# Kernel optimization log

Measured on AMD Instinct MI355X. Metric: run time of the kernel, lower is better.

The kernel has to match this reference:

```python
import jax, jax.numpy as jnp
import numpy as np

N = 100_000   # number of sparse points
C = 128       # channels
K3 = 27       # 3x3x3 kernel offsets


def sparse_conv(x, nbr, W, b):
    """Minkowski-style sparse conv: gather-GEMM-scatter.
    x:   [N, Cin] point features
    nbr: [N, K3] neighbor index per kernel offset; index N -> missing (zero row)
    W:   [K3, Cin, Cout], b: [Cout]
    """
    x_pad = jnp.concatenate([x, jnp.zeros((1, x.shape[1]), x.dtype)], axis=0)

    def step(acc, wk_nk):
        Wk, nk = wk_nk                      # Wk: [Cin,Cout], nk: [N]
        return acc + x_pad[nk] @ Wk, None   # gather + GEMM, accumulate

    acc0 = jnp.broadcast_to(b, (x.shape[0], W.shape[2])).astype(x.dtype)
    acc, _ = jax.lax.scan(step, acc0, (W, nbr.T))
    return acc


def setup_inputs() -> dict:
    key = jax.random.key(0)
    ks = jax.random.split(key, 12)
    Ch = C // 2

    def w(k, shape, fan_in):
        return jax.random.normal(k, shape, dtype=jnp.float32) / np.sqrt(fan_in)

    x = jax.random.normal(ks[0], (N, C), dtype=jnp.float32)
    # neighbor map; value N means "no neighbor" (maps to zero-padded row)
    nbr = jax.random.randint(ks[1], (N, K3), 0, N + 1, dtype=jnp.int32)

    return {
        "x": x,
        "nbr": nbr,
        "W00": w(ks[2], (K3, C, Ch), K3 * C),   # conv0_0: kxkxk, C -> C/2
        "b00": jnp.zeros((Ch,), jnp.float32),
        "W01": w(ks[3], (K3, Ch, Ch), K3 * Ch),  # conv0_1: kxkxk, C/2 -> C/2
        "b01": jnp.zeros((Ch,), jnp.float32),
        "W10": w(ks[4], (C, Ch), C),             # conv1_0: 1x1x1, C -> C/2
        "b10": jnp.zeros((Ch,), jnp.float32),
        "W11": w(ks[5], (K3, Ch, Ch), K3 * Ch),  # conv1_1: kxkxk, C/2 -> C/2
        "b11": jnp.zeros((Ch,), jnp.float32),
        "W12": w(ks[6], (Ch, Ch), Ch),           # conv1_2: 1x1x1, C/2 -> C/2
        "b12": jnp.zeros((Ch,), jnp.float32),
    }


def reference(x, nbr, W00, b00, W01, b01, W10, b10, W11, b11, W12, b12):
    # branch 0: conv -> relu -> conv
    h0 = jax.nn.relu(sparse_conv(x, nbr, W00, b00))
    out0 = sparse_conv(h0, nbr, W01, b01)
    # branch 1: 1x1 conv -> relu -> conv -> relu -> 1x1 conv
    h1 = jax.nn.relu(x @ W10 + b10)
    h1 = jax.nn.relu(sparse_conv(h1, nbr, W11, b11))
    out1 = h1 @ W12 + b12
    # concat channels, residual add
    return jnp.concatenate([out0, out1], axis=1) + x
```

## Files before the change

kernel.cpp:

```cpp
#include <hip/hip_runtime.h>
#include <hip/hip_bf16.h>
#include <stdint.h>

typedef __bf16 bf16x8 __attribute__((ext_vector_type(8)));
typedef float  f32x4  __attribute__((ext_vector_type(4)));

#define MFMA(A, B, C) __builtin_amdgcn_mfma_f32_16x16x32_bf16((A), (B), (C), 0, 0, 0)

#define LDS_BARRIER() asm volatile("s_waitcnt lgkmcnt(0)\n\ts_barrier" ::: "memory")

static __device__ __forceinline__ unsigned short f2b(float f) {
    union { float f; unsigned int u; } v; v.f = f;
    return (unsigned short)((v.u + 0x7FFFu + ((v.u >> 16) & 1u)) >> 16);
}

__global__ __launch_bounds__(256) void convert_kernel(
    const float* __restrict__ x, unsigned short* __restrict__ xb,
    unsigned short* __restrict__ hb, int N) {
    long long i = (long long)blockIdx.x * blockDim.x + threadIdx.x;
    long long base = i * 4;
    long long nx = (long long)N * 128;
    long long total = nx + 128;
    if (base >= total) return;
    if (base < nx) {
        float4 v = *(const float4*)(x + base);
        ushort4 o;
        o.x = f2b(v.x); o.y = f2b(v.y); o.z = f2b(v.z); o.w = f2b(v.w);
        *(ushort4*)(xb + base) = o;
    } else {
        ushort4 z = make_ushort4(0, 0, 0, 0);
        *(ushort4*)(xb + base) = z;
        *(ushort4*)(hb + base) = z;
    }
}

__global__ __launch_bounds__(256) void pack_kernel(
    const float* __restrict__ W00, const float* __restrict__ W01,
    const float* __restrict__ W10, const float* __restrict__ W11,
    const float* __restrict__ W12,
    unsigned short* __restrict__ wp00, unsigned short* __restrict__ wpC,
    unsigned short* __restrict__ wp10, unsigned short* __restrict__ wp12) {
    int g = blockIdx.x * blockDim.x + threadIdx.x;
    const float* W; int cinSteps; int which;
    if (g < 27648)      { W = W00; cinSteps = 4; which = 0; }
    else if (g < 41472) { g -= 27648; W = W01; cinSteps = 2; which = 1; }
    else if (g < 55296) { g -= 41472; W = W11; cinSteps = 2; which = 2; }
    else if (g < 56320) { g -= 55296; W = W10; cinSteps = 4; which = 3; }
    else if (g < 56832) { g -= 56320; W = W12; cinSteps = 2; which = 4; }
    else return;
    int lane = g & 63;
    int st   = g >> 6;
    int t    = st & 3;
    int s    = st >> 2;
    int q = lane >> 4, n16 = lane & 15;
    int k    = s / cinSteps;
    int cinb = (s % cinSteps) * 32;
    int Cin  = cinSteps * 32;
    int cout = t * 16 + n16;
    unsigned short o[8];
#pragma unroll
    for (int j = 0; j < 8; ++j) {
        float v = W[(size_t)(k * Cin + cinb + q * 8 + j) * 64 + cout];
        o[j] = f2b(v);
    }
    unsigned short* dst;
    if (which == 0)      dst = wp00 + (size_t)g * 8;
    else if (which == 1) dst = wpC + (size_t)k * 8192 +
                               ((size_t)(((s & 1) * 4 + t) * 64 + lane)) * 8;
    else if (which == 2) dst = wpC + (size_t)k * 8192 + 4096 +
                               ((size_t)(((s & 1) * 4 + t) * 64 + lane)) * 8;
    else if (which == 3) dst = wp10 + (size_t)g * 8;
    else                 dst = wp12 + (size_t)g * 8;
    *(ushort4*)(dst)     = make_ushort4(o[0], o[1], o[2], o[3]);
    *(ushort4*)(dst + 4) = make_ushort4(o[4], o[5], o[6], o[7]);
}

__global__ __launch_bounds__(256, 3) void passB_kernel(
    const unsigned short* __restrict__ xb, const int* __restrict__ nbr,
    const unsigned short* __restrict__ wp00, const unsigned short* __restrict__ wp10,
    const float* __restrict__ b00, const float* __restrict__ b10,
    unsigned short* __restrict__ hb, int N) {
    __shared__ __align__(16) unsigned short bbuf[2][4096];
    __shared__ __align__(16) int lds_idx[128 * 27];
    const int tid  = threadIdx.x;
    const int lane = tid & 63;
    const int wv   = tid >> 6;
    const int q = lane >> 4, n16 = lane & 15;
    const int rowbase = blockIdx.x * 128 + wv * 32;

    f32x4 acc0[2][4];
    f32x4 acc1[2][4];
#pragma unroll
    for (int rs = 0; rs < 2; ++rs)
#pragma unroll
        for (int t = 0; t < 4; ++t) { acc0[rs][t] = (f32x4)0.f; acc1[rs][t] = (f32x4)0.f; }

    int idxb[2], own[2];
#pragma unroll
    for (int rs = 0; rs < 2; ++rs) {
        idxb[rs] = (wv * 32 + rs * 16 + n16) * 27;
        own[rs]  = min(rowbase + rs * 16 + n16, N - 1);
    }

#pragma unroll
    for (int ph = 0; ph < 2; ++ph) {
        const int choff = ph * 64;
        int4 br[2];
#pragma unroll
        for (int j = 0; j < 2; ++j)
            br[j] = *(const int4*)(wp00 + ph * 4096 + j * 2048 + tid * 8);
        if (ph == 0) {
            long long gbase = (long long)blockIdx.x * 128 * 27;
            long long lim = (long long)N * 27 - 1;
            for (int i = tid; i < 3456; i += 256) {
                long long gi = gbase + i; if (gi > lim) gi = lim;
                lds_idx[i] = nbr[gi];
            }
        }
#pragma unroll
        for (int j = 0; j < 2; ++j) *(int4*)(&bbuf[0][j * 2048 + tid * 8]) = br[j];
        __syncthreads();

        bf16x8 Da[2][2], Db[2][2], Dc[2][2];
#pragma unroll
        for (int rs = 0; rs < 2; ++rs) {
            const unsigned short* p0 =
                xb + (size_t)lds_idx[idxb[rs] + 0] * 128 + choff + q * 8;
            Da[rs][0] = *(const bf16x8*)(p0);
            Da[rs][1] = *(const bf16x8*)(p0 + 32);
            const unsigned short* p1 =
                xb + (size_t)lds_idx[idxb[rs] + 1] * 128 + choff + q * 8;
            Db[rs][0] = *(const bf16x8*)(p1);
            Db[rs][1] = *(const bf16x8*)(p1 + 32);
        }

        for (int k = 0; k < 27; ++k) {
            int buf = k & 1;
            if (k < 26) {
                const unsigned short* src = wp00 + ph * 4096 + (size_t)(k + 1) * 8192;
#pragma unroll
                for (int j = 0; j < 2; ++j)
                    br[j] = *(const int4*)(src + j * 2048 + tid * 8);
            }
#pragma unroll
            for (int rs = 0; rs < 2; ++rs) {
                int j2 = k + 2;
                int ii = (j2 < 27) ? lds_idx[idxb[rs] + j2] : own[rs];
                const unsigned short* p = xb + (size_t)ii * 128 + choff + q * 8;
                Dc[rs][0] = *(const bf16x8*)(p);
                Dc[rs][1] = *(const bf16x8*)(p + 32);
            }
            const unsigned short* lb = &bbuf[buf][0];
#pragma unroll
            for (int s2 = 0; s2 < 2; ++s2) {
#pragma unroll
                for (int t = 0; t < 4; ++t) {
                    bf16x8 B = *(const bf16x8*)(lb + (s2 * 4 + t) * 512 + lane * 8);
#pragma unroll
                    for (int rs = 0; rs < 2; ++rs)
                        acc0[rs][t] = MFMA(Da[rs][s2], B, acc0[rs][t]);
                }
            }
            if (k < 26) {
#pragma unroll
                for (int j = 0; j < 2; ++j)
                    *(int4*)(&bbuf[buf ^ 1][j * 2048 + tid * 8]) = br[j];
            }
#pragma unroll
            for (int rs = 0; rs < 2; ++rs)
#pragma unroll
                for (int s2 = 0; s2 < 2; ++s2) {
                    Da[rs][s2] = Db[rs][s2]; Db[rs][s2] = Dc[rs][s2];
                }
            LDS_BARRIER();
        }

#pragma unroll
        for (int s2 = 0; s2 < 2; ++s2) {
#pragma unroll
            for (int t = 0; t < 4; ++t) {
                bf16x8 B = *(const bf16x8*)(wp10 + ((ph * 2 + s2) * 4 + t) * 512 + lane * 8);
#pragma unroll
                for (int rs = 0; rs < 2; ++rs)
                    acc1[rs][t] = MFMA(Da[rs][s2], B, acc1[rs][t]);
            }
        }
    }

#pragma unroll
    for (int rs = 0; rs < 2; ++rs)
#pragma unroll
        for (int t = 0; t < 4; ++t) {
            int col = t * 16 + n16;
            float bb0 = b00[col], bb1 = b10[col];
#pragma unroll
            for (int r = 0; r < 4; ++r) {
                int row = rowbase + rs * 16 + q * 4 + r;
                if (row < N) {
                    hb[(size_t)row * 128 + col]      = f2b(fmaxf(acc0[rs][t][r] + bb0, 0.f));
                    hb[(size_t)row * 128 + 64 + col] = f2b(fmaxf(acc1[rs][t][r] + bb1, 0.f));
                }
            }
        }
}

__global__ __launch_bounds__(256, 3) void passC_kernel(
    const unsigned short* __restrict__ hb, const int* __restrict__ nbr,
    const float* __restrict__ x,
    const unsigned short* __restrict__ wpC, const unsigned short* __restrict__ wp12,
    const float* __restrict__ b01, const float* __restrict__ b11,
    const float* __restrict__ b12, float* __restrict__ out, int N) {
    __shared__ __align__(16) unsigned short bbuf[2][4096];
    __shared__ __align__(16) int lds_idx[128 * 27];
    const int tid  = threadIdx.x;
    const int lane = tid & 63;
    const int wv   = tid >> 6;
    const int q = lane >> 4, n16 = lane & 15;
    const int rowbase = blockIdx.x * 128 + wv * 32;

    int idxb[2];
#pragma unroll
    for (int rs = 0; rs < 2; ++rs) idxb[rs] = (wv * 32 + rs * 16 + n16) * 27;

    {
        int4 br[2];
#pragma unroll
        for (int j = 0; j < 2; ++j) br[j] = *(const int4*)(wpC + j * 2048 + tid * 8);
        {
            long long gbase = (long long)blockIdx.x * 128 * 27;
            long long lim = (long long)N * 27 - 1;
            for (int i = tid; i < 3456; i += 256) {
                long long gi = gbase + i; if (gi > lim) gi = lim;
                lds_idx[i] = nbr[gi];
            }
        }
#pragma unroll
        for (int j = 0; j < 2; ++j) *(int4*)(&bbuf[0][j * 2048 + tid * 8]) = br[j];
        __syncthreads();

        f32x4 accA[2][4];
#pragma unroll
        for (int rs = 0; rs < 2; ++rs)
#pragma unroll
            for (int t = 0; t < 4; ++t) accA[rs][t] = (f32x4)0.f;

        bf16x8 Da[2][2], Db[2][2], Dc[2][2];
#pragma unroll
        for (int rs = 0; rs < 2; ++rs) {
            const unsigned short* p0 = hb + (size_t)lds_idx[idxb[rs] + 0] * 128 + q * 8;
            Da[rs][0] = *(const bf16x8*)(p0);
            Da[rs][1] = *(const bf16x8*)(p0 + 32);
            const unsigned short* p1 = hb + (size_t)lds_idx[idxb[rs] + 1] * 128 + q * 8;
            Db[rs][0] = *(const bf16x8*)(p1);
            Db[rs][1] = *(const bf16x8*)(p1 + 32);
        }

        for (int k = 0; k < 27; ++k) {
            int buf = k & 1;
            if (k < 26) {
                const unsigned short* src = wpC + (size_t)(k + 1) * 8192;
#pragma unroll
                for (int j = 0; j < 2; ++j)
                    br[j] = *(const int4*)(src + j * 2048 + tid * 8);
            }
#pragma unroll
            for (int rs = 0; rs < 2; ++rs) {
                int j2 = min(k + 2, 26);
                const unsigned short* p =
                    hb + (size_t)lds_idx[idxb[rs] + j2] * 128 + q * 8;
                Dc[rs][0] = *(const bf16x8*)(p);
                Dc[rs][1] = *(const bf16x8*)(p + 32);
            }
            const unsigned short* lb = &bbuf[buf][0];
#pragma unroll
            for (int s2 = 0; s2 < 2; ++s2) {
#pragma unroll
                for (int t = 0; t < 4; ++t) {
                    bf16x8 B = *(const bf16x8*)(lb + (s2 * 4 + t) * 512 + lane * 8);
#pragma unroll
                    for (int rs = 0; rs < 2; ++rs)
                        accA[rs][t] = MFMA(Da[rs][s2], B, accA[rs][t]);
                }
            }
            if (k < 26) {
#pragma unroll
                for (int j = 0; j < 2; ++j)
                    *(int4*)(&bbuf[buf ^ 1][j * 2048 + tid * 8]) = br[j];
            }
#pragma unroll
            for (int rs = 0; rs < 2; ++rs)
#pragma unroll
                for (int s2 = 0; s2 < 2; ++s2) {
                    Da[rs][s2] = Db[rs][s2]; Db[rs][s2] = Dc[rs][s2];
                }
            LDS_BARRIER();
        }

#pragma unroll
        for (int rs = 0; rs < 2; ++rs)
#pragma unroll
            for (int t = 0; t < 4; ++t) {
                int col = t * 16 + n16;
                float bo = b01[col];
#pragma unroll
                for (int r = 0; r < 4; ++r) {
                    int row = rowbase + rs * 16 + q * 4 + r;
                    if (row < N) {
                        float xv = __builtin_nontemporal_load(x + (size_t)row * 128 + col);
                        __builtin_nontemporal_store(accA[rs][t][r] + bo + xv,
                                                    out + (size_t)row * 128 + col);
                    }
                }
            }
    }

    {
        int4 br[2];
#pragma unroll
        for (int j = 0; j < 2; ++j)
            br[j] = *(const int4*)(wpC + 4096 + j * 2048 + tid * 8);
#pragma unroll
        for (int j = 0; j < 2; ++j) *(int4*)(&bbuf[0][j * 2048 + tid * 8]) = br[j];
        __syncthreads();

        f32x4 accT[2][4];
#pragma unroll
        for (int rs = 0; rs < 2; ++rs)
#pragma unroll
            for (int t = 0; t < 4; ++t) accT[rs][t] = (f32x4)0.f;

        bf16x8 Da[2][2], Db[2][2], Dc[2][2];
#pragma unroll
        for (int rs = 0; rs < 2; ++rs) {
            const unsigned short* p0 =
                hb + (size_t)lds_idx[idxb[rs] + 0] * 128 + 64 + q * 8;
            Da[rs][0] = *(const bf16x8*)(p0);
            Da[rs][1] = *(const bf16x8*)(p0 + 32);
            const unsigned short* p1 =
                hb + (size_t)lds_idx[idxb[rs] + 1] * 128 + 64 + q * 8;
            Db[rs][0] = *(const bf16x8*)(p1);
            Db[rs][1] = *(const bf16x8*)(p1 + 32);
        }

        for (int k = 0; k < 27; ++k) {
            int buf = k & 1;
            if (k < 26) {
                const unsigned short* src = wpC + 4096 + (size_t)(k + 1) * 8192;
#pragma unroll
                for (int j = 0; j < 2; ++j)
                    br[j] = *(const int4*)(src + j * 2048 + tid * 8);
            }
#pragma unroll
            for (int rs = 0; rs < 2; ++rs) {
                int j2 = min(k + 2, 26);
                const unsigned short* p =
                    hb + (size_t)lds_idx[idxb[rs] + j2] * 128 + 64 + q * 8;
                Dc[rs][0] = *(const bf16x8*)(p);
                Dc[rs][1] = *(const bf16x8*)(p + 32);
            }
            const unsigned short* lb = &bbuf[buf][0];
#pragma unroll
            for (int s2 = 0; s2 < 2; ++s2) {
#pragma unroll
                for (int t = 0; t < 4; ++t) {
                    bf16x8 B = *(const bf16x8*)(lb + (s2 * 4 + t) * 512 + lane * 8);
#pragma unroll
                    for (int rs = 0; rs < 2; ++rs)
                        accT[rs][t] = MFMA(Da[rs][s2], B, accT[rs][t]);
                }
            }
            if (k < 26) {
#pragma unroll
                for (int j = 0; j < 2; ++j)
                    *(int4*)(&bbuf[buf ^ 1][j * 2048 + tid * 8]) = br[j];
            }
#pragma unroll
            for (int rs = 0; rs < 2; ++rs)
#pragma unroll
                for (int s2 = 0; s2 < 2; ++s2) {
                    Da[rs][s2] = Db[rs][s2]; Db[rs][s2] = Dc[rs][s2];
                }
            LDS_BARRIER();
        }

        unsigned short* myl = (wv < 3) ? ((unsigned short*)lds_idx + wv * 2304)
                                       : &bbuf[0][0];
#pragma unroll
        for (int rs = 0; rs < 2; ++rs)
#pragma unroll
            for (int t = 0; t < 4; ++t) {
                int col = t * 16 + n16;
                float bt = b11[col];
#pragma unroll
                for (int r = 0; r < 4; ++r) {
                    float tv = fmaxf(accT[rs][t][r] + bt, 0.f);
                    myl[(rs * 16 + q * 4 + r) * 72 + col] = f2b(tv);
                }
            }

        f32x4 accO1[2][4];
#pragma unroll
        for (int rs = 0; rs < 2; ++rs)
#pragma unroll
            for (int t = 0; t < 4; ++t) accO1[rs][t] = (f32x4)0.f;
#pragma unroll
        for (int s2 = 0; s2 < 2; ++s2) {
#pragma unroll
            for (int t = 0; t < 4; ++t) {
                bf16x8 B = *(const bf16x8*)(wp12 + s2 * 2048 + t * 512 + lane * 8);
#pragma unroll
                for (int rs = 0; rs < 2; ++rs) {
                    bf16x8 A = *(const bf16x8*)(myl + (rs * 16 + n16) * 72 + s2 * 32 + q * 8);
                    accO1[rs][t] = MFMA(A, B, accO1[rs][t]);
                }
            }
        }
#pragma unroll
        for (int rs = 0; rs < 2; ++rs)
#pragma unroll
            for (int t = 0; t < 4; ++t) {
                int col = t * 16 + n16;
                float bo = b12[col];
#pragma unroll
                for (int r = 0; r < 4; ++r) {
                    int row = rowbase + rs * 16 + q * 4 + r;
                    if (row < N) {
                        float xv = __builtin_nontemporal_load(x + (size_t)row * 128 + 64 + col);
                        __builtin_nontemporal_store(accO1[rs][t][r] + bo + xv,
                                                    out + (size_t)row * 128 + 64 + col);
                    }
                }
            }
    }
}

extern "C" void kernel_launch(void* const* d_in, const int* in_sizes, int n_in,
                              void* d_out, int out_size, void* d_ws, size_t ws_size,
                              hipStream_t stream) {
    const float* x   = (const float*)d_in[0];
    const int*   nbr = (const int*)d_in[1];
    const float* W00 = (const float*)d_in[2];
    const float* b00 = (const float*)d_in[3];
    const float* W01 = (const float*)d_in[4];
    const float* b01 = (const float*)d_in[5];
    const float* W10 = (const float*)d_in[6];
    const float* b10 = (const float*)d_in[7];
    const float* W11 = (const float*)d_in[8];
    const float* b11 = (const float*)d_in[9];
    const float* W12 = (const float*)d_in[10];
    const float* b12 = (const float*)d_in[11];
    float* out = (float*)d_out;
    int N = in_sizes[0] / 128;

    char* ws = (char*)d_ws;
    size_t cur = 0;
    unsigned short* xb  = (unsigned short*)(ws + cur); cur += (size_t)(N + 1) * 128 * 2;
    unsigned short* hb  = (unsigned short*)(ws + cur); cur += (size_t)(N + 1) * 128 * 2;
    unsigned short* wp00 = (unsigned short*)(ws + cur); cur += 27648 * 8 * 2;
    unsigned short* wpC  = (unsigned short*)(ws + cur); cur += (size_t)27 * 8192 * 2;
    unsigned short* wp10 = (unsigned short*)(ws + cur); cur += 8192 * 2;
    unsigned short* wp12 = (unsigned short*)(ws + cur); cur += 4096 * 2;

    long long cvt_groups = ((long long)N * 128 + 128) / 4;
    int cvt_blocks = (int)((cvt_groups + 255) / 256);
    convert_kernel<<<cvt_blocks, 256, 0, stream>>>(x, xb, hb, N);
    pack_kernel<<<222, 256, 0, stream>>>(W00, W01, W10, W11, W12,
                                         wp00, wpC, wp10, wp12);
    int nstrips = (N + 127) / 128;
    passB_kernel<<<nstrips, 256, 0, stream>>>(xb, nbr, wp00, wp10, b00, b10, hb, N);
    passC_kernel<<<nstrips, 256, 0, stream>>>(hb, nbr, x, wpC, wp12,
                                              b01, b11, b12, out, N);
}
```

Before: 417.8 us.

## Widen passB tiles to 256 rows and full 128 channels in one pass

passB now processes 256 rows per block, 64 per wave, and covers all 128 input channels in a single k-loop instead of two 64-channel phases. Each gathered neighbor row is read once at full width, and each weight slice is staged once per block for twice as many rows. The gather prefetch depth drops from two offsets ahead to one. Register use rises (16 accumulators of each kind plus 32 fragment vectors), so occupancy is lowered to 2 blocks per CU, and the block count halves, which may hurt latency hiding.

```diff
diff --git a/kernel.cpp b/kernel.cpp
--- a/kernel.cpp
+++ b/kernel.cpp
@@ -75,120 +75,107 @@
     *(ushort4*)(dst + 4) = make_ushort4(o[4], o[5], o[6], o[7]);
 }
 
-__global__ __launch_bounds__(256, 3) void passB_kernel(
+__global__ __launch_bounds__(256, 2) void passB_kernel(
     const unsigned short* __restrict__ xb, const int* __restrict__ nbr,
     const unsigned short* __restrict__ wp00, const unsigned short* __restrict__ wp10,
     const float* __restrict__ b00, const float* __restrict__ b10,
     unsigned short* __restrict__ hb, int N) {
-    __shared__ __align__(16) unsigned short bbuf[2][4096];
-    __shared__ __align__(16) int lds_idx[128 * 27];
+    __shared__ __align__(16) unsigned short bbuf[2][8192];
+    __shared__ __align__(16) int lds_idx[256 * 27];
     const int tid  = threadIdx.x;
     const int lane = tid & 63;
     const int wv   = tid >> 6;
     const int q = lane >> 4, n16 = lane & 15;
-    const int rowbase = blockIdx.x * 128 + wv * 32;
-
-    f32x4 acc0[2][4];
-    f32x4 acc1[2][4];
-#pragma unroll
-    for (int rs = 0; rs < 2; ++rs)
+    const int rowbase = blockIdx.x * 256 + wv * 64;
+
+    int4 br[4];
+#pragma unroll
+    for (int j = 0; j < 4; ++j) br[j] = *(const int4*)(wp00 + j * 2048 + tid * 8);
+    {
+        long long gbase = (long long)blockIdx.x * 256 * 27;
+        long long lim = (long long)N * 27 - 1;
+        for (int i = tid; i < 6912; i += 256) {
+            long long gi = gbase + i; if (gi > lim) gi = lim;
+            lds_idx[i] = nbr[gi];
+        }
+    }
+#pragma unroll
+    for (int j = 0; j < 4; ++j) *(int4*)(&bbuf[0][j * 2048 + tid * 8]) = br[j];
+    __syncthreads();
+
+    f32x4 acc0[4][4];
+    f32x4 acc1[4][4];
+#pragma unroll
+    for (int rs = 0; rs < 4; ++rs)
 #pragma unroll
         for (int t = 0; t < 4; ++t) { acc0[rs][t] = (f32x4)0.f; acc1[rs][t] = (f32x4)0.f; }
 
-    int idxb[2], own[2];
-#pragma unroll
-    for (int rs = 0; rs < 2; ++rs) {
-        idxb[rs] = (wv * 32 + rs * 16 + n16) * 27;
+    int idxb[4], own[4];
+#pragma unroll
+    for (int rs = 0; rs < 4; ++rs) {
+        idxb[rs] = (wv * 64 + rs * 16 + n16) * 27;
         own[rs]  = min(rowbase + rs * 16 + n16, N - 1);
     }
 
-#pragma unroll
-    for (int ph = 0; ph < 2; ++ph) {
-        const int choff = ph * 64;
-        int4 br[2];
-#pragma unroll
-        for (int j = 0; j < 2; ++j)
-            br[j] = *(const int4*)(wp00 + ph * 4096 + j * 2048 + tid * 8);
-        if (ph == 0) {
-            long long gbase = (long long)blockIdx.x * 128 * 27;
-            long long lim = (long long)N * 27 - 1;
-            for (int i = tid; i < 3456; i += 256) {
-                long long gi = gbase + i; if (gi > lim) gi = lim;
-                lds_idx[i] = nbr[gi];
-            }
-        }
-#pragma unroll
-        for (int j = 0; j < 2; ++j) *(int4*)(&bbuf[0][j * 2048 + tid * 8]) = br[j];
-        __syncthreads();
-
-        bf16x8 Da[2][2], Db[2][2], Dc[2][2];
-#pragma unroll
-        for (int rs = 0; rs < 2; ++rs) {
-            const unsigned short* p0 =
-                xb + (size_t)lds_idx[idxb[rs] + 0] * 128 + choff + q * 8;
-            Da[rs][0] = *(const bf16x8*)(p0);
-            Da[rs][1] = *(const bf16x8*)(p0 + 32);
-            const unsigned short* p1 =
-                xb + (size_t)lds_idx[idxb[rs] + 1] * 128 + choff + q * 8;
-            Db[rs][0] = *(const bf16x8*)(p1);
-            Db[rs][1] = *(const bf16x8*)(p1 + 32);
-        }
-
-        for (int k = 0; k < 27; ++k) {
-            int buf = k & 1;
-            if (k < 26) {
-                const unsigned short* src = wp00 + ph * 4096 + (size_t)(k + 1) * 8192;
-#pragma unroll
-                for (int j = 0; j < 2; ++j)
-                    br[j] = *(const int4*)(src + j * 2048 + tid * 8);
-            }
-#pragma unroll
-            for (int rs = 0; rs < 2; ++rs) {
-                int j2 = k + 2;
-                int ii = (j2 < 27) ? lds_idx[idxb[rs] + j2] : own[rs];
-                const unsigned short* p = xb + (size_t)ii * 128 + choff + q * 8;
-                Dc[rs][0] = *(const bf16x8*)(p);
-                Dc[rs][1] = *(const bf16x8*)(p + 32);
-            }
-            const unsigned short* lb = &bbuf[buf][0];
-#pragma unroll
-            for (int s2 = 0; s2 < 2; ++s2) {
-#pragma unroll
-                for (int t = 0; t < 4; ++t) {
-                    bf16x8 B = *(const bf16x8*)(lb + (s2 * 4 + t) * 512 + lane * 8);
-#pragma unroll
-                    for (int rs = 0; rs < 2; ++rs)
-                        acc0[rs][t] = MFMA(Da[rs][s2], B, acc0[rs][t]);
-                }
-            }
-            if (k < 26) {
-#pragma unroll
-                for (int j = 0; j < 2; ++j)
-                    *(int4*)(&bbuf[buf ^ 1][j * 2048 + tid * 8]) = br[j];
-            }
-#pragma unroll
-            for (int rs = 0; rs < 2; ++rs)
-#pragma unroll
-                for (int s2 = 0; s2 < 2; ++s2) {
-                    Da[rs][s2] = Db[rs][s2]; Db[rs][s2] = Dc[rs][s2];
-                }
-            LDS_BARRIER();
-        }
-
-#pragma unroll
-        for (int s2 = 0; s2 < 2; ++s2) {
+    bf16x8 D[4][4];
+#pragma unroll
+    for (int rs = 0; rs < 4; ++rs) {
+        const unsigned short* p = xb + (size_t)lds_idx[idxb[rs]] * 128 + q * 8;
+#pragma unroll
+        for (int s2 = 0; s2 < 4; ++s2) D[rs][s2] = *(const bf16x8*)(p + s2 * 32);
+    }
+
+    for (int k = 0; k < 27; ++k) {
+        int buf = k & 1;
+        if (k < 26) {
+            const unsigned short* src = wp00 + (size_t)(k + 1) * 8192;
+#pragma unroll
+            for (int j = 0; j < 4; ++j) br[j] = *(const int4*)(src + j * 2048 + tid * 8);
+        }
+        bf16x8 Dn[4][4];
+#pragma unroll
+        for (int rs = 0; rs < 4; ++rs) {
+            int ian = (k + 1 < 27) ? lds_idx[idxb[rs] + k + 1] : own[rs];
+            const unsigned short* p = xb + (size_t)ian * 128 + q * 8;
+#pragma unroll
+            for (int s2 = 0; s2 < 4; ++s2) Dn[rs][s2] = *(const bf16x8*)(p + s2 * 32);
+        }
+        const unsigned short* lb = &bbuf[buf][0];
+#pragma unroll
+        for (int s2 = 0; s2 < 4; ++s2) {
 #pragma unroll
             for (int t = 0; t < 4; ++t) {
-                bf16x8 B = *(const bf16x8*)(wp10 + ((ph * 2 + s2) * 4 + t) * 512 + lane * 8);
-#pragma unroll
-                for (int rs = 0; rs < 2; ++rs)
-                    acc1[rs][t] = MFMA(Da[rs][s2], B, acc1[rs][t]);
-            }
-        }
-    }
-
-#pragma unroll
-    for (int rs = 0; rs < 2; ++rs)
+                bf16x8 B = *(const bf16x8*)(lb + (s2 * 4 + t) * 512 + lane * 8);
+#pragma unroll
+                for (int rs = 0; rs < 4; ++rs)
+                    acc0[rs][t] = MFMA(D[rs][s2], B, acc0[rs][t]);
+            }
+        }
+        if (k < 26) {
+#pragma unroll
+            for (int j = 0; j < 4; ++j)
+                *(int4*)(&bbuf[buf ^ 1][j * 2048 + tid * 8]) = br[j];
+        }
+#pragma unroll
+        for (int rs = 0; rs < 4; ++rs)
+#pragma unroll
+            for (int s2 = 0; s2 < 4; ++s2) D[rs][s2] = Dn[rs][s2];
+        LDS_BARRIER();
+    }
+
+#pragma unroll
+    for (int s2 = 0; s2 < 4; ++s2) {
+#pragma unroll
+        for (int t = 0; t < 4; ++t) {
+            bf16x8 B = *(const bf16x8*)(wp10 + s2 * 2048 + t * 512 + lane * 8);
+#pragma unroll
+            for (int rs = 0; rs < 4; ++rs)
+                acc1[rs][t] = MFMA(D[rs][s2], B, acc1[rs][t]);
+        }
+    }
+
+#pragma unroll
+    for (int rs = 0; rs < 4; ++rs)
 #pragma unroll
         for (int t = 0; t < 4; ++t) {
             int col = t * 16 + n16;
@@ -466,8 +453,9 @@
     convert_kernel<<<cvt_blocks, 256, 0, stream>>>(x, xb, hb, N);
     pack_kernel<<<222, 256, 0, stream>>>(W00, W01, W10, W11, W12,
                                          wp00, wpC, wp10, wp12);
-    int nstrips = (N + 127) / 128;
-    passB_kernel<<<nstrips, 256, 0, stream>>>(xb, nbr, wp00, wp10, b00, b10, hb, N);
-    passC_kernel<<<nstrips, 256, 0, stream>>>(hb, nbr, x, wpC, wp12,
-                                              b01, b11, b12, out, N);
-}
+    int nstripsB = (N + 255) / 256;
+    passB_kernel<<<nstripsB, 256, 0, stream>>>(xb, nbr, wp00, wp10, b00, b10, hb, N);
+    int nstripsC = (N + 127) / 128;
+    passC_kernel<<<nstripsC, 256, 0, stream>>>(hb, nbr, x, wpC, wp12,
+                                               b01, b11, b12, out, N);
+}
```

Result: faster. 393.1 us (-5.9%).
